# Optimization experiments

Hardware: AMD Instinct MI355X
Metric: run time of the kernel (lower is better)

The kernel has to match this reference:

```python
import jax, jax.numpy as jnp
import numpy as np

VOCAB, EMB, K = 100000, 128, 11
SIGMA = 0.1
EPS = 1e-8


def setup_inputs() -> dict:
    key = jax.random.key(0)
    k1, k2, k3, k4, k5 = jax.random.split(key, 5)
    queries = jax.random.randint(k1, (128, 16), 0, VOCAB)
    documents = jax.random.randint(k2, (128, 2048), 0, VOCAB)
    emb_table = jax.random.normal(k3, (VOCAB, EMB), dtype=jnp.float32)
    emb_table = emb_table.at[0].set(0.0)  # padding_idx=0
    W = jax.random.normal(k4, (1, K), dtype=jnp.float32)
    b = jax.random.normal(k5, (1,), dtype=jnp.float32)
    return {"queries": queries, "documents": documents, "emb_table": emb_table, "W": W, "b": b}


def reference(queries, documents, emb_table, W, b):
    mus = jnp.arange(-1.0, 1.1, 2.0 / (K - 1), dtype=jnp.float32)  # 11 kernel centers
    q = emb_table[queries]          # (B, Q, E)
    d = emb_table[documents]        # (B, L, E)
    dot = jnp.einsum('bqe,ble->bql', q, d)
    qn = jnp.linalg.norm(q, axis=-1, keepdims=True)          # (B, Q, 1)
    dn = jnp.linalg.norm(d, axis=-1, keepdims=True)          # (B, L, 1)
    sim = dot / (qn * jnp.swapaxes(dn, 1, 2) + EPS)          # (B, Q, L)
    rbf = jnp.exp(-(sim[..., None] - mus) ** 2 / (2.0 * SIGMA ** 2))  # (B, Q, L, K)
    pooled = rbf.sum(axis=2)                                  # (B, Q, K)
    soft_tf = jnp.log(pooled).sum(axis=1)                     # (B, K)
    return jax.nn.sigmoid(soft_tf @ W.T + b)                  # (B, 1)
```

## Files before the change

### kernel.cpp

```cpp
#include <hip/hip_runtime.h>

typedef _Float16 half8  __attribute__((ext_vector_type(8)));
typedef float    floatx4 __attribute__((ext_vector_type(4)));

#define KNRM_VOCAB 100000


__global__ __launch_bounds__(256) void knrm_convert(
    const float* __restrict__ emb, _Float16* __restrict__ tab)
{
    const int row = blockIdx.x * 16 + (threadIdx.x >> 4);
    const int sub = threadIdx.x & 15;
    const float4* src = (const float4*)(emb + (size_t)row * 128 + sub * 8);
    const float4 v0 = src[0], v1 = src[1];
    float ns = v0.x*v0.x + v0.y*v0.y + v0.z*v0.z + v0.w*v0.w
             + v1.x*v1.x + v1.y*v1.y + v1.z*v1.z + v1.w*v1.w;
    ns += __shfl_xor(ns, 1); ns += __shfl_xor(ns, 2);
    ns += __shfl_xor(ns, 4); ns += __shfl_xor(ns, 8);
    const float inv = ns > 0.0f ? 1.0f / sqrtf(ns) : 0.0f;
    half8 h;
    h[0] = (_Float16)(v0.x*inv); h[1] = (_Float16)(v0.y*inv);
    h[2] = (_Float16)(v0.z*inv); h[3] = (_Float16)(v0.w*inv);
    h[4] = (_Float16)(v1.x*inv); h[5] = (_Float16)(v1.y*inv);
    h[6] = (_Float16)(v1.z*inv); h[7] = (_Float16)(v1.w*inv);
    *(half8*)(tab + (size_t)row * 128 + sub * 8) = h;
}

__global__ __launch_bounds__(256, 4) void knrm_main_h(
    const int*      __restrict__ queries,
    const int*      __restrict__ documents,
    const _Float16* __restrict__ tab,
    float*          __restrict__ partials)
{
    const int tid  = threadIdx.x;
    const int b    = blockIdx.x >> 3;
    const int tok0 = (blockIdx.x & 7) * 256;
    const int lane = tid & 63;
    const int wave = tid >> 6;
    const int col  = lane & 15;
    const int quad = lane >> 4;

    const int qi = queries[b * 16 + col];
    const _Float16* qp = tab + (size_t)qi * 128 + quad * 8;
    half8 qf[4];
#pragma unroll
    for (int c = 0; c < 4; ++c) qf[c] = *(const half8*)(qp + c * 32);

    int idx[4];
#pragma unroll
    for (int t = 0; t < 4; ++t)
        idx[t] = documents[b * 2048 + tok0 + (t * 4 + wave) * 16 + col];

    half8 d[4][4];
#pragma unroll
    for (int t = 0; t < 4; ++t) {
        const _Float16* rp = tab + (size_t)idx[t] * 128 + quad * 8;
#pragma unroll
        for (int c = 0; c < 4; ++c) d[t][c] = *(const half8*)(rp + c * 32);
    }

    float pr[11];
#pragma unroll
    for (int k = 0; k < 11; ++k) pr[k] = 0.0f;

#pragma unroll
    for (int t = 0; t < 4; ++t) {
        floatx4 acc = {0.0f, 0.0f, 0.0f, 0.0f};
#pragma unroll
        for (int c = 0; c < 4; ++c)
            acc = __builtin_amdgcn_mfma_f32_16x16x32_f16(d[t][c], qf[c], acc, 0, 0, 0);

#pragma unroll
        for (int r = 0; r < 4; ++r) {
            const float s = acc[r];
#pragma unroll
            for (int k = 0; k < 11; ++k) {
                const float tt = s - (-1.0f + 0.2f * (float)k);
                pr[k] += __builtin_amdgcn_exp2f(tt * tt * -72.13475204444817f);
            }
        }
    }

#pragma unroll
    for (int k = 0; k < 11; ++k) {
        pr[k] += __shfl_xor(pr[k], 16);
        pr[k] += __shfl_xor(pr[k], 32);
    }

    __shared__ float ps[4][176];
    if (lane < 16) {
#pragma unroll
        for (int k = 0; k < 11; ++k) ps[wave][col * 11 + k] = pr[k];
    }
    __syncthreads();
    if (tid < 176)
        partials[blockIdx.x * 176 + tid] =
            ps[0][tid] + ps[1][tid] + ps[2][tid] + ps[3][tid];
}

__global__ __launch_bounds__(192) void knrm_final_h(
    const float* __restrict__ partials,
    const float* __restrict__ W,
    const float* __restrict__ bias,
    float*       __restrict__ out)
{
    const int b = blockIdx.x, t = threadIdx.x;
    float v = 0.0f;
    if (t < 176) {
        float s = 0.0f;
#pragma unroll
        for (int c = 0; c < 8; ++c) s += partials[(b * 8 + c) * 176 + t];
        const int k = t - (t / 11) * 11;
        v = __builtin_amdgcn_logf(s) * 0.69314718055994531f * W[k];
    }
#pragma unroll
    for (int off = 1; off < 64; off <<= 1) v += __shfl_xor(v, off);
    __shared__ float red[3];
    if ((t & 63) == 0) red[t >> 6] = v;
    __syncthreads();
    if (t == 0) {
        const float a = red[0] + red[1] + red[2] + bias[0];
        out[b] = __builtin_amdgcn_rcpf(1.0f + __builtin_amdgcn_exp2f(a * -1.4426950408889634f));
    }
}


__global__ __launch_bounds__(256) void knrm_zero(float* __restrict__ p) {
    p[blockIdx.x * 256 + threadIdx.x] = 0.0f;
}

__global__ __launch_bounds__(256) void knrm_main(
    const int*   __restrict__ queries,
    const int*   __restrict__ documents,
    const float* __restrict__ emb,
    float*       __restrict__ pooled)
{
    __shared__ __align__(16) _Float16 Qs[16][136];
    __shared__ float qn_s[16];
    __shared__ float pooled_s[176];

    const int tid  = threadIdx.x;
    const int b    = blockIdx.x >> 3;
    const int tok0 = (blockIdx.x & 7) * 256;

    {
        const int row = tid >> 4, sub = tid & 15;
        const int qi = queries[b * 16 + row];
        const float4* src = (const float4*)(emb + (size_t)qi * 128 + sub * 8);
        float4 v0 = src[0], v1 = src[1];
        half8 h;
        h[0] = (_Float16)v0.x; h[1] = (_Float16)v0.y;
        h[2] = (_Float16)v0.z; h[3] = (_Float16)v0.w;
        h[4] = (_Float16)v1.x; h[5] = (_Float16)v1.y;
        h[6] = (_Float16)v1.z; h[7] = (_Float16)v1.w;
        *(half8*)&Qs[row][sub * 8] = h;
        float ns = v0.x*v0.x + v0.y*v0.y + v0.z*v0.z + v0.w*v0.w
                 + v1.x*v1.x + v1.y*v1.y + v1.z*v1.z + v1.w*v1.w;
        ns += __shfl_xor(ns, 1); ns += __shfl_xor(ns, 2);
        ns += __shfl_xor(ns, 4); ns += __shfl_xor(ns, 8);
        if (sub == 0) qn_s[row] = sqrtf(ns);
    }
    if (tid < 176) pooled_s[tid] = 0.0f;
    __syncthreads();

    const int lane = tid & 63;
    const int wave = tid >> 6;
    const int col  = lane & 15;
    const int quad = lane >> 4;

    half8 afrag[4];
#pragma unroll
    for (int c = 0; c < 4; ++c)
        afrag[c] = *(const half8*)&Qs[col][c * 32 + quad * 8];

    float pr[4][11];
#pragma unroll
    for (int r = 0; r < 4; ++r)
#pragma unroll
        for (int k = 0; k < 11; ++k) pr[r][k] = 0.0f;

    int idx[4];
#pragma unroll
    for (int j = 0; j < 4; ++j)
        idx[j] = documents[b * 2048 + tok0 + (j * 4 + wave) * 16 + col];

    float4 cur[8];
    {
        const float* rp = emb + (size_t)idx[0] * 128 + quad * 8;
#pragma unroll
        for (int c = 0; c < 4; ++c) {
            cur[2*c]   = *(const float4*)(rp + c * 32);
            cur[2*c+1] = *(const float4*)(rp + c * 32 + 4);
        }
    }

    for (int j = 0; j < 4; ++j) {
        float4 nxt[8];
        if (j < 3) {
            const float* rp = emb + (size_t)idx[j + 1] * 128 + quad * 8;
#pragma unroll
            for (int c = 0; c < 4; ++c) {
                nxt[2*c]   = *(const float4*)(rp + c * 32);
                nxt[2*c+1] = *(const float4*)(rp + c * 32 + 4);
            }
        }

        half8 bf[4];
        float ns = 0.0f;
#pragma unroll
        for (int c = 0; c < 4; ++c) {
            float4 a = cur[2*c], dd = cur[2*c+1];
            half8 h;
            h[0] = (_Float16)a.x; h[1] = (_Float16)a.y;
            h[2] = (_Float16)a.z; h[3] = (_Float16)a.w;
            h[4] = (_Float16)dd.x; h[5] = (_Float16)dd.y;
            h[6] = (_Float16)dd.z; h[7] = (_Float16)dd.w;
            bf[c] = h;
            ns += a.x*a.x + a.y*a.y + a.z*a.z + a.w*a.w
                + dd.x*dd.x + dd.y*dd.y + dd.z*dd.z + dd.w*dd.w;
        }
        ns += __shfl_xor(ns, 16);
        ns += __shfl_xor(ns, 32);
        const float dn = sqrtf(ns);

        floatx4 acc = {0.0f, 0.0f, 0.0f, 0.0f};
#pragma unroll
        for (int c = 0; c < 4; ++c)
            acc = __builtin_amdgcn_mfma_f32_16x16x32_f16(afrag[c], bf[c], acc, 0, 0, 0);

#pragma unroll
        for (int r = 0; r < 4; ++r) {
            const float denom = qn_s[quad * 4 + r] * dn + 1e-8f;
            const float sim = acc[r] * __builtin_amdgcn_rcpf(denom);
#pragma unroll
            for (int k = 0; k < 11; ++k) {
                const float tt = sim - (-1.0f + 0.2f * (float)k);
                pr[r][k] += __builtin_amdgcn_exp2f(tt * tt * -72.13475204444817f);
            }
        }

#pragma unroll
        for (int i = 0; i < 8; ++i) cur[i] = nxt[i];
    }

#pragma unroll
    for (int r = 0; r < 4; ++r)
#pragma unroll
        for (int k = 0; k < 11; ++k)
            atomicAdd(&pooled_s[(quad * 4 + r) * 11 + k], pr[r][k]);
    __syncthreads();
    if (tid < 176) atomicAdd(&pooled[b * 176 + tid], pooled_s[tid]);
}

__global__ __launch_bounds__(128) void knrm_final(
    const float* __restrict__ pooled,
    const float* __restrict__ W,
    const float* __restrict__ bias,
    float*       __restrict__ out)
{
    const int b = threadIdx.x;
    float acc = bias[0];
#pragma unroll
    for (int k = 0; k < 11; ++k) {
        float s = 0.0f;
#pragma unroll
        for (int q = 0; q < 16; ++q)
            s += __builtin_amdgcn_logf(pooled[b * 176 + q * 11 + k]);
        acc += s * 0.69314718055994531f * W[k];
    }
    out[b] = __builtin_amdgcn_rcpf(1.0f + __builtin_amdgcn_exp2f(acc * -1.4426950408889634f));
}


extern "C" void kernel_launch(void* const* d_in, const int* in_sizes, int n_in,
                              void* d_out, int out_size, void* d_ws, size_t ws_size,
                              hipStream_t stream) {
    const int*   queries   = (const int*)d_in[0];
    const int*   documents = (const int*)d_in[1];
    const float* emb       = (const float*)d_in[2];
    const float* W         = (const float*)d_in[3];
    const float* bias      = (const float*)d_in[4];
    float* out = (float*)d_out;

    const size_t TABB = (size_t)KNRM_VOCAB * 128 * sizeof(_Float16);
    const size_t NEED = TABB + (size_t)1024 * 176 * sizeof(float);

    if (ws_size >= NEED) {
        _Float16* tab      = (_Float16*)d_ws;
        float*    partials = (float*)((char*)d_ws + TABB);
        knrm_convert<<<6250, 256, 0, stream>>>(emb, tab);
        knrm_main_h<<<1024, 256, 0, stream>>>(queries, documents, tab, partials);
        knrm_final_h<<<128, 192, 0, stream>>>(partials, W, bias, out);
    } else {
        float* pooled = (float*)d_ws;
        knrm_zero<<<88, 256, 0, stream>>>(pooled);
        knrm_main<<<1024, 256, 0, stream>>>(queries, documents, emb, pooled);
        knrm_final<<<1, 128, 0, stream>>>(pooled, W, bias, out);
    }
}
```

Measured before the change: 110.0 us.

## Quantize normalized embedding table to int8 and use i8 MFMA

The fp16 normalized table is replaced by an int8 table quantized per row, plus a per-row float scale that also folds in the L2 normalization. The main kernel gathers half as many bytes per row and computes dots with the i8 16x16x64 MFMA, rescaling by both scales before the RBF kernels. This cuts the conversion write traffic and the gather read traffic. The cost is lower similarity precision, which the narrow RBF kernels (sigma 0.1) could amplify enough to exceed tolerance.

New measurement: 106.4 us. 3.3% less time.

```diff
diff --git a/kernel.cpp b/kernel.cpp
--- a/kernel.cpp
+++ b/kernel.cpp
@@ -2,12 +2,15 @@
 
 typedef _Float16 half8  __attribute__((ext_vector_type(8)));
 typedef float    floatx4 __attribute__((ext_vector_type(4)));
+typedef int      intx4  __attribute__((ext_vector_type(4)));
+typedef char     char8  __attribute__((ext_vector_type(8)));
 
 #define KNRM_VOCAB 100000
 
 
-__global__ __launch_bounds__(256) void knrm_convert(
-    const float* __restrict__ emb, _Float16* __restrict__ tab)
+__global__ __launch_bounds__(256) void knrm_convert_i8(
+    const float* __restrict__ emb, char* __restrict__ tab,
+    float* __restrict__ scales)
 {
     const int row = blockIdx.x * 16 + (threadIdx.x >> 4);
     const int sub = threadIdx.x & 15;
@@ -15,22 +18,30 @@
     const float4 v0 = src[0], v1 = src[1];
     float ns = v0.x*v0.x + v0.y*v0.y + v0.z*v0.z + v0.w*v0.w
              + v1.x*v1.x + v1.y*v1.y + v1.z*v1.z + v1.w*v1.w;
+    float mx = fmaxf(fmaxf(fmaxf(fabsf(v0.x), fabsf(v0.y)), fmaxf(fabsf(v0.z), fabsf(v0.w))),
+                     fmaxf(fmaxf(fabsf(v1.x), fabsf(v1.y)), fmaxf(fabsf(v1.z), fabsf(v1.w))));
     ns += __shfl_xor(ns, 1); ns += __shfl_xor(ns, 2);
     ns += __shfl_xor(ns, 4); ns += __shfl_xor(ns, 8);
-    const float inv = ns > 0.0f ? 1.0f / sqrtf(ns) : 0.0f;
-    half8 h;
-    h[0] = (_Float16)(v0.x*inv); h[1] = (_Float16)(v0.y*inv);
-    h[2] = (_Float16)(v0.z*inv); h[3] = (_Float16)(v0.w*inv);
-    h[4] = (_Float16)(v1.x*inv); h[5] = (_Float16)(v1.y*inv);
-    h[6] = (_Float16)(v1.z*inv); h[7] = (_Float16)(v1.w*inv);
-    *(half8*)(tab + (size_t)row * 128 + sub * 8) = h;
-}
-
-__global__ __launch_bounds__(256, 4) void knrm_main_h(
-    const int*      __restrict__ queries,
-    const int*      __restrict__ documents,
-    const _Float16* __restrict__ tab,
-    float*          __restrict__ partials)
+    mx = fmaxf(mx, __shfl_xor(mx, 1)); mx = fmaxf(mx, __shfl_xor(mx, 2));
+    mx = fmaxf(mx, __shfl_xor(mx, 4)); mx = fmaxf(mx, __shfl_xor(mx, 8));
+    const bool nz = (ns > 0.0f);
+    const float qm = nz ? 127.0f / mx : 0.0f;
+    const float s  = nz ? mx / (127.0f * sqrtf(ns)) : 0.0f;
+    char8 q;
+    q[0] = (char)(int)rintf(v0.x * qm); q[1] = (char)(int)rintf(v0.y * qm);
+    q[2] = (char)(int)rintf(v0.z * qm); q[3] = (char)(int)rintf(v0.w * qm);
+    q[4] = (char)(int)rintf(v1.x * qm); q[5] = (char)(int)rintf(v1.y * qm);
+    q[6] = (char)(int)rintf(v1.z * qm); q[7] = (char)(int)rintf(v1.w * qm);
+    *(char8*)(tab + (size_t)row * 128 + sub * 8) = q;
+    if (sub == 0) scales[row] = s;
+}
+
+__global__ __launch_bounds__(256, 4) void knrm_main_i8(
+    const int*   __restrict__ queries,
+    const int*   __restrict__ documents,
+    const char*  __restrict__ tab,
+    const float* __restrict__ scales,
+    float*       __restrict__ partials)
 {
     const int tid  = threadIdx.x;
     const int b    = blockIdx.x >> 3;
@@ -41,22 +52,25 @@
     const int quad = lane >> 4;
 
     const int qi = queries[b * 16 + col];
-    const _Float16* qp = tab + (size_t)qi * 128 + quad * 8;
-    half8 qf[4];
-#pragma unroll
-    for (int c = 0; c < 4; ++c) qf[c] = *(const half8*)(qp + c * 32);
+    const float sq = scales[qi];
+    const intx4* qp = (const intx4*)(tab + (size_t)qi * 128);
+    intx4 qf[2];
+#pragma unroll
+    for (int c = 0; c < 2; ++c) qf[c] = qp[c * 4 + quad];
 
     int idx[4];
 #pragma unroll
     for (int t = 0; t < 4; ++t)
         idx[t] = documents[b * 2048 + tok0 + (t * 4 + wave) * 16 + col];
 
-    half8 d[4][4];
+    intx4 d[4][2];
+    float sdl[4];
 #pragma unroll
     for (int t = 0; t < 4; ++t) {
-        const _Float16* rp = tab + (size_t)idx[t] * 128 + quad * 8;
-#pragma unroll
-        for (int c = 0; c < 4; ++c) d[t][c] = *(const half8*)(rp + c * 32);
+        const intx4* rp = (const intx4*)(tab + (size_t)idx[t] * 128);
+#pragma unroll
+        for (int c = 0; c < 2; ++c) d[t][c] = rp[c * 4 + quad];
+        sdl[t] = scales[idx[t]];
     }
 
     float pr[11];
@@ -65,14 +79,15 @@
 
 #pragma unroll
     for (int t = 0; t < 4; ++t) {
-        floatx4 acc = {0.0f, 0.0f, 0.0f, 0.0f};
-#pragma unroll
-        for (int c = 0; c < 4; ++c)
-            acc = __builtin_amdgcn_mfma_f32_16x16x32_f16(d[t][c], qf[c], acc, 0, 0, 0);
+        intx4 acc = {0, 0, 0, 0};
+#pragma unroll
+        for (int c = 0; c < 2; ++c)
+            acc = __builtin_amdgcn_mfma_i32_16x16x64_i8(d[t][c], qf[c], acc, 0, 0, 0);
 
 #pragma unroll
         for (int r = 0; r < 4; ++r) {
-            const float s = acc[r];
+            const float sd = __shfl(sdl[t], quad * 4 + r);
+            const float s = (float)acc[r] * sd * sq;
 #pragma unroll
             for (int k = 0; k < 11; ++k) {
                 const float tt = s - (-1.0f + 0.2f * (float)k);
@@ -282,14 +297,16 @@
     const float* bias      = (const float*)d_in[4];
     float* out = (float*)d_out;
 
-    const size_t TABB = (size_t)KNRM_VOCAB * 128 * sizeof(_Float16);
-    const size_t NEED = TABB + (size_t)1024 * 176 * sizeof(float);
+    const size_t TABB = (size_t)KNRM_VOCAB * 128;
+    const size_t SCLB = (size_t)KNRM_VOCAB * sizeof(float);
+    const size_t NEED = TABB + SCLB + (size_t)1024 * 176 * sizeof(float);
 
     if (ws_size >= NEED) {
-        _Float16* tab      = (_Float16*)d_ws;
-        float*    partials = (float*)((char*)d_ws + TABB);
-        knrm_convert<<<6250, 256, 0, stream>>>(emb, tab);
-        knrm_main_h<<<1024, 256, 0, stream>>>(queries, documents, tab, partials);
+        char*  tab      = (char*)d_ws;
+        float* scales   = (float*)((char*)d_ws + TABB);
+        float* partials = (float*)((char*)d_ws + TABB + SCLB);
+        knrm_convert_i8<<<6250, 256, 0, stream>>>(emb, tab, scales);
+        knrm_main_i8<<<1024, 256, 0, stream>>>(queries, documents, tab, scales, partials);
         knrm_final_h<<<128, 192, 0, stream>>>(partials, W, bias, out);
     } else {
         float* pooled = (float*)d_ws;
```
